# Kernel tuning notes

Measured on AMD Instinct MI355X. Metric: run time of the kernel, lower is better.

The kernel has to match this reference:

```python
import jax, jax.numpy as jnp
import numpy as np

POOL = 7      # AdaptiveMaxPool2d output size
CROP = 96     # max box side; all generated boxes fit inside a CROP x CROP window


def _adaptive_maxpool_box(feature_chw, coord):
    """PyTorch AdaptiveMaxPool2d((7,7)) on feature_chw[:, y1:y2, x1:x2].

    feature_chw: [2, H, W]; coord: int32 [4] = (y1, x1, y2, x2), with
    0 < y2-y1 <= CROP, 0 < x2-x1 <= CROP. Returns [2, 7, 7].
    """
    y1, x1, y2, x2 = coord[0], coord[1], coord[2], coord[3]
    crop = jax.lax.dynamic_slice(feature_chw, (0, y1, x1), (2, CROP, CROP))
    h = y2 - y1
    w = x2 - x1
    i = jnp.arange(POOL)
    r = jnp.arange(CROP)
    # PyTorch adaptive pooling bins: [floor(i*h/P), ceil((i+1)*h/P))
    sr = (i * h) // POOL
    er = ((i + 1) * h + POOL - 1) // POOL
    sc = (i * w) // POOL
    ec = ((i + 1) * w + POOL - 1) // POOL
    mask_r = (r[None, :] >= sr[:, None]) & (r[None, :] < er[:, None])  # [7, CROP]
    mask_c = (r[None, :] >= sc[:, None]) & (r[None, :] < ec[:, None])  # [7, CROP]
    neg = jnp.finfo(crop.dtype).min
    # row-wise max per output row: [7, 2, CROP]
    rowp = jnp.max(jnp.where(mask_r[:, None, :, None], crop[None], neg), axis=2)
    # col-wise max per output col: [7, 7, 2]
    out = jnp.max(jnp.where(mask_c[None, :, None, :], rowp[:, None], neg), axis=3)
    return jnp.transpose(out, (2, 0, 1))  # [2, 7, 7]


def setup_inputs() -> dict:
    key = jax.random.key(0)
    k1, k2, k3, k4, k5, k6 = jax.random.split(key, 6)
    N = 1024
    H = W = 2048
    feature = jax.random.normal(k1, (1, 2, H, W), jnp.float32)
    y1 = jax.random.randint(k2, (N,), 0, H - CROP)
    x1 = jax.random.randint(k3, (N,), 0, W - CROP)
    hh = jax.random.randint(k4, (N,), POOL, CROP)
    ww = jax.random.randint(k5, (N,), POOL, CROP)
    box_coords = jnp.stack([y1, x1, y1 + hh, x1 + ww], axis=1).astype(jnp.int32)
    boxes = jnp.concatenate(
        [jnp.zeros((N, 1), jnp.float32),
         jnp.arange(N, dtype=jnp.float32)[:, None],
         box_coords.astype(jnp.float32)], axis=1)  # [N, 6]
    fc_w = jax.random.normal(k6, (4, POOL * POOL * 2), jnp.float32) * 0.1
    fc_b = jnp.zeros((4,), jnp.float32)
    return {"feature": feature, "boxes": boxes, "box_coords": box_coords,
            "fc_w": fc_w, "fc_b": fc_b}


def reference(feature, boxes, box_coords, fc_w, fc_b):
    # per-box ROI adaptive max pool, batched with vmap: [N, 2, 7, 7]
    pooled = jax.vmap(lambda c: _adaptive_maxpool_box(feature[0], c))(box_coords)
    feat = pooled.reshape(pooled.shape[0], -1)        # [N, 98] (channel-major flatten)
    deltaB = jax.nn.relu(feat @ fc_w.T + fc_b)        # [N, 4]
    return boxes.at[:, 2:6].add(deltaB)               # boxes[:,2:6] += deltaB
```

## Files before the change

### kernel.cpp

```cpp
#include <hip/hip_runtime.h>
#include <float.h>

#define POOL 7
#define FW 2048
#define FH 2048
#define CROP 96
#define LROW 100

__global__ __launch_bounds__(256, 4) void roi_pool_fc_kernel(
    const float* __restrict__ feature,
    const float* __restrict__ boxes,
    const int*   __restrict__ coords,
    const float* __restrict__ fc_w,
    const float* __restrict__ fc_b,
    float* __restrict__ out,
    int N)
{
    const int n = blockIdx.x;
    const int t = threadIdx.x;

    __shared__ float lds[CROP * LROW];
    __shared__ float pooled[98];
    __shared__ float delta[4];

    const int y1 = coords[n * 4 + 0];
    const int x1 = coords[n * 4 + 1];
    const int h  = coords[n * 4 + 2] - y1;
    const int w  = coords[n * 4 + 3] - x1;

    const int x1a  = x1 & ~3;
    const int off  = x1 - x1a;
    const int wvec = (w + off + 3) >> 2;

    const int o = t >> 2;
    const int s = t & 3;
    const int i = o / 7;
    const int j = o % 7;
    int sr = 0, er = 0, sc = 0, ec = 0, sc4 = 0, ec4 = 0;
    if (t < 196) {
        sr  = (i * h) / POOL;
        er  = ((i + 1) * h + POOL - 1) / POOL;
        sc  = (j * w) / POOL + off;
        ec  = ((j + 1) * w + POOL - 1) / POOL + off;
        sc4 = sc >> 2;
        ec4 = (ec + 3) >> 2;
    }

    const float* b0 = feature + (size_t)y1 * FW + x1a;
    const float* b1 = b0 + (size_t)FH * FW;

    float4 regs[10];
    int vrow[10], vc4[10];
    bool vok[10];
    #pragma unroll
    for (int k = 0; k < 10; ++k) {
        const int v = t + k * 256;
        const int r = v / 25;
        vrow[k] = r;
        vc4[k]  = v - r * 25;
        vok[k]  = (v < 2400) && (r < h) && (vc4[k] < wvec);
        regs[k] = vok[k] ? ((const float4*)(b0 + (size_t)r * FW))[vc4[k]]
                         : make_float4(0.f, 0.f, 0.f, 0.f);
    }
    #pragma unroll
    for (int k = 0; k < 10; ++k)
        if (vok[k]) ((float4*)&lds[vrow[k] * LROW])[vc4[k]] = regs[k];
    __syncthreads();

    #pragma unroll
    for (int k = 0; k < 10; ++k)
        regs[k] = vok[k] ? ((const float4*)(b1 + (size_t)vrow[k] * FW))[vc4[k]]
                         : make_float4(0.f, 0.f, 0.f, 0.f);

    if (t < 196) {
        float m = -FLT_MAX;
        for (int r = sr + s; r < er; r += 4) {
            const float4* rowp = (const float4*)(lds + r * LROW);
            for (int c4 = sc4; c4 < ec4; ++c4) {
                const float4 v = rowp[c4];
                const int b = c4 * 4;
                m = fmaxf(m, (b + 0 >= sc && b + 0 < ec) ? v.x : -FLT_MAX);
                m = fmaxf(m, (b + 1 >= sc && b + 1 < ec) ? v.y : -FLT_MAX);
                m = fmaxf(m, (b + 2 >= sc && b + 2 < ec) ? v.z : -FLT_MAX);
                m = fmaxf(m, (b + 3 >= sc && b + 3 < ec) ? v.w : -FLT_MAX);
            }
        }
        m = fmaxf(m, __shfl_xor(m, 1, 64));
        m = fmaxf(m, __shfl_xor(m, 2, 64));
        if (s == 0) pooled[o] = m;
    }
    __syncthreads();

    #pragma unroll
    for (int k = 0; k < 10; ++k)
        if (vok[k]) ((float4*)&lds[vrow[k] * LROW])[vc4[k]] = regs[k];
    __syncthreads();

    if (t < 196) {
        float m = -FLT_MAX;
        for (int r = sr + s; r < er; r += 4) {
            const float4* rowp = (const float4*)(lds + r * LROW);
            for (int c4 = sc4; c4 < ec4; ++c4) {
                const float4 v = rowp[c4];
                const int b = c4 * 4;
                m = fmaxf(m, (b + 0 >= sc && b + 0 < ec) ? v.x : -FLT_MAX);
                m = fmaxf(m, (b + 1 >= sc && b + 1 < ec) ? v.y : -FLT_MAX);
                m = fmaxf(m, (b + 2 >= sc && b + 2 < ec) ? v.z : -FLT_MAX);
                m = fmaxf(m, (b + 3 >= sc && b + 3 < ec) ? v.w : -FLT_MAX);
            }
        }
        m = fmaxf(m, __shfl_xor(m, 1, 64));
        m = fmaxf(m, __shfl_xor(m, 2, 64));
        if (s == 0) pooled[49 + o] = m;
    }
    __syncthreads();

    if (t < 128) {
        const int oo   = t >> 5;
        const int lane = t & 31;
        const float* wrow = fc_w + oo * 98;
        float acc = 0.f;
        #pragma unroll
        for (int k = lane; k < 98; k += 32)
            acc = fmaf(pooled[k], wrow[k], acc);
        #pragma unroll
        for (int m = 16; m; m >>= 1)
            acc += __shfl_xor(acc, m, 64);
        if (lane == 0) delta[oo] = fmaxf(acc + fc_b[oo], 0.f);
    }
    __syncthreads();

    if (t < 6) {
        float v = boxes[n * 6 + t];
        if (t >= 2) v += delta[t - 2];
        out[n * 6 + t] = v;
    }
}

extern "C" void kernel_launch(void* const* d_in, const int* in_sizes, int n_in,
                              void* d_out, int out_size, void* d_ws, size_t ws_size,
                              hipStream_t stream) {
    const float* feature = (const float*)d_in[0];
    const float* boxes   = (const float*)d_in[1];
    const int*   coords  = (const int*)d_in[2];
    const float* fc_w    = (const float*)d_in[3];
    const float* fc_b    = (const float*)d_in[4];
    float* out = (float*)d_out;

    const int N = in_sizes[2] / 4;
    roi_pool_fc_kernel<<<N, 256, 0, stream>>>(feature, boxes, coords, fc_w, fc_b, out, N);
}
```

Baseline: 85.09 us.

## Load first channel straight into LDS and prefetch FC weights, bias and boxes

The first feature channel now uses the AMD global_load_lds builtin to copy tiles from global memory straight into LDS, skipping the register round trip and LDS store. The LDS layout is the same as before. The second channel's register loads are issued right after, together with the first channel's. The box coordinates are read as one int4, and the FC weights, bias and box values are loaded before pooling so their latency is hidden. A risk: the wait before the barrier may also wait for the second channel's loads, which could reduce the overlap between loading and compute.

```diff
diff --git a/kernel.cpp b/kernel.cpp
--- a/kernel.cpp
+++ b/kernel.cpp
@@ -6,6 +6,10 @@
 #define FH 2048
 #define CROP 96
 #define LROW 100
+
+#define GLD16(gp, lp) __builtin_amdgcn_global_load_lds( \
+    (const __attribute__((address_space(1))) void*)(gp), \
+    (__attribute__((address_space(3))) void*)(lp), 16, 0, 0)
 
 __global__ __launch_bounds__(256, 4) void roi_pool_fc_kernel(
     const float* __restrict__ feature,
@@ -23,14 +27,55 @@
     __shared__ float pooled[98];
     __shared__ float delta[4];
 
-    const int y1 = coords[n * 4 + 0];
-    const int x1 = coords[n * 4 + 1];
-    const int h  = coords[n * 4 + 2] - y1;
-    const int w  = coords[n * 4 + 3] - x1;
+    const int4 cd = ((const int4*)coords)[n];
+    const int y1 = cd.x;
+    const int x1 = cd.y;
+    const int h  = cd.z - y1;
+    const int w  = cd.w - x1;
 
     const int x1a  = x1 & ~3;
     const int off  = x1 - x1a;
     const int wvec = (w + off + 3) >> 2;
+
+    float wpre[4] = {0.f, 0.f, 0.f, 0.f};
+    float bias = 0.f;
+    if (t < 128) {
+        const int oo = t >> 5, lane = t & 31;
+        const float* wrow = fc_w + oo * 98;
+        #pragma unroll
+        for (int k = 0; k < 4; ++k) {
+            const int idx = lane + 32 * k;
+            if (idx < 98) wpre[k] = wrow[idx];
+        }
+        if (lane == 0) bias = fc_b[oo];
+    }
+    const float bx = (t < 6) ? boxes[n * 6 + t] : 0.f;
+
+    const float* b0 = feature + (size_t)y1 * FW + x1a;
+    const float* b1 = b0 + (size_t)FH * FW;
+    const int wbase = t & 192;
+
+    int   goff[10];
+    bool  vok[10];
+    #pragma unroll
+    for (int k = 0; k < 10; ++k) {
+        const int v = t + k * 256;
+        const int r = v / 25;
+        const int c4 = v - r * 25;
+        goff[k] = r * FW + 4 * c4;
+        vok[k]  = (v < 2400) && (r < h) && (c4 < wvec);
+    }
+
+    #pragma unroll
+    for (int k = 0; k < 10; ++k) {
+        char* lbase = (char*)lds + 16 * (wbase + k * 256);
+        if (vok[k]) GLD16(b0 + goff[k], lbase);
+    }
+    float4 regs[10];
+    #pragma unroll
+    for (int k = 0; k < 10; ++k)
+        regs[k] = vok[k] ? *(const float4*)(b1 + goff[k])
+                         : make_float4(0.f, 0.f, 0.f, 0.f);
 
     const int o = t >> 2;
     const int s = t & 3;
@@ -46,31 +91,7 @@
         ec4 = (ec + 3) >> 2;
     }
 
-    const float* b0 = feature + (size_t)y1 * FW + x1a;
-    const float* b1 = b0 + (size_t)FH * FW;
-
-    float4 regs[10];
-    int vrow[10], vc4[10];
-    bool vok[10];
-    #pragma unroll
-    for (int k = 0; k < 10; ++k) {
-        const int v = t + k * 256;
-        const int r = v / 25;
-        vrow[k] = r;
-        vc4[k]  = v - r * 25;
-        vok[k]  = (v < 2400) && (r < h) && (vc4[k] < wvec);
-        regs[k] = vok[k] ? ((const float4*)(b0 + (size_t)r * FW))[vc4[k]]
-                         : make_float4(0.f, 0.f, 0.f, 0.f);
-    }
-    #pragma unroll
-    for (int k = 0; k < 10; ++k)
-        if (vok[k]) ((float4*)&lds[vrow[k] * LROW])[vc4[k]] = regs[k];
     __syncthreads();
-
-    #pragma unroll
-    for (int k = 0; k < 10; ++k)
-        regs[k] = vok[k] ? ((const float4*)(b1 + (size_t)vrow[k] * FW))[vc4[k]]
-                         : make_float4(0.f, 0.f, 0.f, 0.f);
 
     if (t < 196) {
         float m = -FLT_MAX;
@@ -93,7 +114,7 @@
 
     #pragma unroll
     for (int k = 0; k < 10; ++k)
-        if (vok[k]) ((float4*)&lds[vrow[k] * LROW])[vc4[k]] = regs[k];
+        if (vok[k]) *(float4*)((char*)lds + 16 * (t + k * 256)) = regs[k];
     __syncthreads();
 
     if (t < 196) {
@@ -116,25 +137,22 @@
     __syncthreads();
 
     if (t < 128) {
-        const int oo   = t >> 5;
         const int lane = t & 31;
-        const float* wrow = fc_w + oo * 98;
         float acc = 0.f;
         #pragma unroll
-        for (int k = lane; k < 98; k += 32)
-            acc = fmaf(pooled[k], wrow[k], acc);
+        for (int k = 0; k < 4; ++k) {
+            const int idx = lane + 32 * k;
+            acc = fmaf(idx < 98 ? pooled[idx] : 0.f, wpre[k], acc);
+        }
         #pragma unroll
-        for (int m = 16; m; m >>= 1)
-            acc += __shfl_xor(acc, m, 64);
-        if (lane == 0) delta[oo] = fmaxf(acc + fc_b[oo], 0.f);
+        for (int mm = 16; mm; mm >>= 1)
+            acc += __shfl_xor(acc, mm, 64);
+        if (lane == 0) delta[t >> 5] = fmaxf(acc + bias, 0.f);
     }
     __syncthreads();
 
-    if (t < 6) {
-        float v = boxes[n * 6 + t];
-        if (t >= 2) v += delta[t - 2];
-        out[n * 6 + t] = v;
-    }
+    if (t < 6)
+        out[n * 6 + t] = bx + (t >= 2 ? delta[t - 2] : 0.f);
 }
 
 extern "C" void kernel_launch(void* const* d_in, const int* in_sizes, int n_in,
```

New measurement: 85.60 us. Within noise of the previous version (+0.6%).
